# Performance work log

Hardware: AMD Instinct MI355X
Metric: run time of the kernel (lower is better)

The kernel has to match this reference:

```python
import jax, jax.numpy as jnp
import numpy as np

B, S, D, H = 2, 2048, 1024, 16
HD = D // H


def setup_inputs() -> dict:
    key = jax.random.key(0)
    ks = jax.random.split(key, 12)
    s = 1.0 / np.sqrt(D)
    inp = {
        "queries": jax.random.normal(ks[0], (B, S, D), jnp.float32),
        "keys": jax.random.normal(ks[1], (B, S, D), jnp.float32),
        "values": jax.random.normal(ks[2], (B, S, D), jnp.float32),
        # True = masked out (causal upper triangle)
        "attn_mask": jnp.triu(jnp.ones((S, S), bool), k=1),
        "W_q": jax.random.normal(ks[3], (D, D), jnp.float32) * s,
        "b_q": jnp.zeros((D,), jnp.float32),
        "W_k": jax.random.normal(ks[4], (D, D), jnp.float32) * s,
        "b_k": jnp.zeros((D,), jnp.float32),
        "W_v": jax.random.normal(ks[5], (D, D), jnp.float32) * s,
        "b_v": jnp.zeros((D,), jnp.float32),
        "W_o": jax.random.normal(ks[6], (D, D), jnp.float32) * s,
        "b_o": jnp.zeros((D,), jnp.float32),
    }
    return inp


def _split_heads(x):
    b, s, _ = x.shape
    return x.reshape(b, s, H, HD).transpose(0, 2, 1, 3)  # (B,H,S,HD)


def reference(queries, keys, values, attn_mask, W_q, b_q, W_k, b_k, W_v, b_v, W_o, b_o):
    Q = _split_heads(queries @ W_q + b_q)
    K = _split_heads(keys @ W_k + b_k)
    V = _split_heads(values @ W_v + b_v)
    scale = 1.0 / np.sqrt(HD)
    scores = jnp.einsum("bhqd,bhkd->bhqk", Q, K) * scale  # (B,H,S,S)
    scores = jnp.where(attn_mask, jnp.float32(-1e9), scores)
    probs = jax.nn.softmax(scores, axis=-1)
    ctx = jnp.einsum("bhqk,bhkd->bhqd", probs, V)
    ctx = ctx.transpose(0, 2, 1, 3).reshape(queries.shape[0], queries.shape[1], D)
    return ctx @ W_o + b_o
```

## Files before the change

kernel.cpp:

```cpp
#include <hip/hip_runtime.h>
#include <hip/hip_bf16.h>
#include <math.h>

typedef __bf16 bf16x8 __attribute__((ext_vector_type(8)));
typedef float f32x4 __attribute__((ext_vector_type(4)));
typedef unsigned short u16x8 __attribute__((ext_vector_type(8)));
typedef unsigned short u16x4 __attribute__((ext_vector_type(4)));

static __device__ __forceinline__ unsigned short f2bf(float f) {
    union { float f; unsigned u; } v; v.f = f;
    unsigned r = v.u + 0x7fffu + ((v.u >> 16) & 1u);
    return (unsigned short)(r >> 16);
}

static __device__ __forceinline__ float exp2fast(float x) {
    return __builtin_exp2f(x);
}

static __device__ __forceinline__ void gload16(const void* g, void* l) {
    __builtin_amdgcn_global_load_lds((const __attribute__((address_space(1))) unsigned int*)g,
                                     (__attribute__((address_space(3))) unsigned int*)l, 16, 0, 0);
}

#define MFMA16(a, b, c) __builtin_amdgcn_mfma_f32_16x16x32_bf16((a), (b), (c), 0, 0, 0)

static __device__ __forceinline__ bf16x8 frag_swz(const unsigned short* base, int row, int chunk) {
    return *(const bf16x8*)((const char*)base + row * 128 + (((chunk ^ row) & 7) << 4));
}

struct Cv3 { const float* in[3]; unsigned short* out[3]; };

__global__ void conv3_kernel(Cv3 a) {
    const int x = blockIdx.x;
    const int sel = x >> 11;
    const size_t i = (((size_t)(x & 2047)) * 256 + threadIdx.x) * 8;
    const float* in = a.in[sel];
    f32x4 v0 = *(const f32x4*)(in + i);
    f32x4 v1 = *(const f32x4*)(in + i + 4);
    u16x8 o;
#pragma unroll
    for (int j = 0; j < 4; ++j) { o[j] = f2bf(v0[j]); o[j + 4] = f2bf(v1[j]); }
    *(u16x8*)(a.out[sel] + i) = o;
}

struct Cw4 { const float* W[4]; unsigned short* Wt[4]; };

__global__ void conv_wt4_kernel(Cw4 a) {
    __shared__ __align__(16) unsigned short Ws[64][66];
    const float* W = a.W[blockIdx.z];
    unsigned short* Wt = a.Wt[blockIdx.z];
    const int t = threadIdx.x;
    const int r0 = blockIdx.y * 64;
    const int c0 = blockIdx.x * 64;
#pragma unroll
    for (int p = 0; p < 4; ++p) {
        int lin = p * 256 + t;
        int r = lin >> 4, cc = (lin & 15) * 4;
        f32x4 v = *(const f32x4*)(W + (size_t)(r0 + r) * 1024 + c0 + cc);
#pragma unroll
        for (int j = 0; j < 4; ++j) Ws[r][cc + j] = f2bf(v[j]);
    }
    __syncthreads();
#pragma unroll
    for (int p = 0; p < 2; ++p) {
        int lin = p * 256 + t;
        int n = lin >> 3, kc = (lin & 7) * 8;
        u16x8 o;
#pragma unroll
        for (int j = 0; j < 8; ++j) o[j] = Ws[kc + j][n];
        *(u16x8*)(Wt + (size_t)(c0 + n) * 1024 + r0 + kc) = o;
    }
}

struct QkvArgs {
    const unsigned short* A[3];
    const unsigned short* Wt[3];
    const float* bias[3];
    unsigned short* out[3];
    float scale[3];
};

__global__ __launch_bounds__(256, 3)
void gemm_qkv(QkvArgs p)
{
    __shared__ __align__(16) unsigned short As[128 * 64];
    __shared__ __align__(16) unsigned short Bs[128 * 64];

    const int z = blockIdx.z;
    const unsigned short* A  = p.A[z];
    const unsigned short* Bt = p.Wt[z];
    const float* bias = p.bias[z];
    unsigned short* out = p.out[z];
    const float oscale = p.scale[z];

    const int t = threadIdx.x, lane = t & 63, w = t >> 6;
    const int lr = lane & 15, lh = lane >> 4;
    const int m0 = blockIdx.y * 128, n0 = blockIdx.x * 128;
    const int wm = (w >> 1) * 64, wn = (w & 1) * 64;
    const int wbase = (t & 0xC0) * 8;

    f32x4 acc[4][4];
#pragma unroll
    for (int i = 0; i < 4; ++i)
#pragma unroll
        for (int j = 0; j < 4; ++j)
#pragma unroll
            for (int e = 0; e < 4; ++e) acc[i][j][e] = 0.0f;

    for (int kt = 0; kt < 16; ++kt) {
        const int k0 = kt << 6;
        __syncthreads();
#pragma unroll
        for (int q = 0; q < 4; ++q) {
            int lin = q * 256 + t;
            int row = lin >> 3, sc = (lin ^ (lin >> 3)) & 7;
            gload16(A + (size_t)(m0 + row) * 1024 + k0 + sc * 8, &As[q * 2048 + wbase]);
        }
#pragma unroll
        for (int q = 0; q < 4; ++q) {
            int lin = q * 256 + t;
            int row = lin >> 3, sc = (lin ^ (lin >> 3)) & 7;
            gload16(Bt + (size_t)(n0 + row) * 1024 + k0 + sc * 8, &Bs[q * 2048 + wbase]);
        }
        __syncthreads();
#pragma unroll
        for (int kb = 0; kb < 2; ++kb) {
            bf16x8 a[4], b[4];
#pragma unroll
            for (int i = 0; i < 4; ++i) a[i] = frag_swz(As, wm + i * 16 + lr, kb * 4 + lh);
#pragma unroll
            for (int j = 0; j < 4; ++j) b[j] = frag_swz(Bs, wn + j * 16 + lr, kb * 4 + lh);
#pragma unroll
            for (int i = 0; i < 4; ++i)
#pragma unroll
                for (int j = 0; j < 4; ++j)
                    acc[i][j] = MFMA16(a[i], b[j], acc[i][j]);
        }
    }

#pragma unroll
    for (int i = 0; i < 4; ++i) {
#pragma unroll
        for (int j = 0; j < 4; ++j) {
            const int gcol = n0 + wn + j * 16 + lr;
            const float bv = bias[gcol];
            const int h_ = gcol >> 6, hd_ = gcol & 63;
            if (z == 2) {
                const int grow0 = m0 + wm + i * 16 + lh * 4;
                const int b_ = grow0 >> 11, s_ = grow0 & 2047;
                u16x4 pk;
#pragma unroll
                for (int r = 0; r < 4; ++r) pk[r] = f2bf((acc[i][j][r] + bv) * oscale);
                *(u16x4*)(out + (((size_t)((b_ * 16 + h_) * 64 + hd_)) << 11) + s_) = pk;
            } else {
#pragma unroll
                for (int r = 0; r < 4; ++r) {
                    const int grow = m0 + wm + i * 16 + lh * 4 + r;
                    const int b_ = grow >> 11, s_ = grow & 2047;
                    out[((size_t)((b_ * 16 + h_) * 2048 + s_) << 6) + hd_] =
                        f2bf((acc[i][j][r] + bv) * oscale);
                }
            }
        }
    }
}

__global__ __launch_bounds__(256, 3)
void gemm_o(const unsigned short* __restrict__ A, const unsigned short* __restrict__ Bt,
            const float* __restrict__ bias, float* __restrict__ Out)
{
    __shared__ __align__(16) unsigned short As[2][64 * 64];
    __shared__ __align__(16) unsigned short Bs[2][128 * 64];

    const int t = threadIdx.x, lane = t & 63, w = t >> 6;
    const int lr = lane & 15, lh = lane >> 4;
    const int m0 = blockIdx.y * 64, n0 = blockIdx.x * 128;
    const int wm = (w >> 1) * 32, wn = (w & 1) * 64;
    const int wbase = (t & 0xC0) * 8;

    f32x4 acc[2][4];
#pragma unroll
    for (int i = 0; i < 2; ++i)
#pragma unroll
        for (int j = 0; j < 4; ++j)
#pragma unroll
            for (int e = 0; e < 4; ++e) acc[i][j][e] = 0.0f;

    auto stage = [&](int buf, int kt) {
        const int k0 = kt << 6;
#pragma unroll
        for (int q = 0; q < 2; ++q) {
            int lin = q * 256 + t;
            int row = lin >> 3, sc = (lin ^ (lin >> 3)) & 7;
            gload16(A + (size_t)(m0 + row) * 1024 + k0 + sc * 8, &As[buf][q * 2048 + wbase]);
        }
#pragma unroll
        for (int q = 0; q < 4; ++q) {
            int lin = q * 256 + t;
            int row = lin >> 3, sc = (lin ^ (lin >> 3)) & 7;
            gload16(Bt + (size_t)(n0 + row) * 1024 + k0 + sc * 8, &Bs[buf][q * 2048 + wbase]);
        }
    };

    stage(0, 0);
    for (int kt = 0; kt < 16; ++kt) {
        __syncthreads();
        if (kt + 1 < 16) stage((kt + 1) & 1, kt + 1);
        const unsigned short* as = As[kt & 1];
        const unsigned short* bs = Bs[kt & 1];
#pragma unroll
        for (int kb = 0; kb < 2; ++kb) {
            bf16x8 a[2], b[4];
#pragma unroll
            for (int i = 0; i < 2; ++i) a[i] = frag_swz(as, wm + i * 16 + lr, kb * 4 + lh);
#pragma unroll
            for (int j = 0; j < 4; ++j) b[j] = frag_swz(bs, wn + j * 16 + lr, kb * 4 + lh);
#pragma unroll
            for (int i = 0; i < 2; ++i)
#pragma unroll
                for (int j = 0; j < 4; ++j)
                    acc[i][j] = MFMA16(a[i], b[j], acc[i][j]);
        }
    }

#pragma unroll
    for (int i = 0; i < 2; ++i) {
#pragma unroll
        for (int j = 0; j < 4; ++j) {
            const int gcol = n0 + wn + j * 16 + lr;
            const float bv = bias[gcol];
#pragma unroll
            for (int r = 0; r < 4; ++r) {
                const int grow = m0 + wm + i * 16 + lh * 4 + r;
                Out[(size_t)grow * 1024 + gcol] = acc[i][j][r] + bv;
            }
        }
    }
}

__global__ __launch_bounds__(256, 2)
void attn_kernel(const unsigned short* __restrict__ Qp,
                 const unsigned short* __restrict__ Kp,
                 const unsigned short* __restrict__ Vtp,
                 unsigned short* __restrict__ Cp)
{
    __shared__ __align__(16) unsigned short Ks[2][64 * 64];
    __shared__ __align__(16) unsigned short Vs[2][64 * 64];
    __shared__ __align__(16) unsigned short Pl[4][16 * 64];

    const int t = threadIdx.x, lane = t & 63, w = t >> 6;
    const int lr = lane & 15, lh = lane >> 4;
    const int wbase = (t & 0xC0) * 8;

    const int g = blockIdx.x;
    const int local = g >> 3;
    const int bh = (g & 7) * 4 + (local >> 4);
    const int qA = local & 15;
    const size_t baseQK = (size_t)bh * (2048 * 64);
    const size_t baseV  = (size_t)bh * (64 * 2048);

    auto stageKV = [&](int buf, int kv0) {
#pragma unroll
        for (int q = 0; q < 2; ++q) {
            int lin = q * 256 + t;
            int row = lin >> 3, sc = (lin ^ (lin >> 3)) & 7;
            gload16(Kp + baseQK + (size_t)(kv0 + row) * 64 + sc * 8, &Ks[buf][q * 2048 + wbase]);
        }
#pragma unroll
        for (int q = 0; q < 2; ++q) {
            int lin = q * 256 + t;
            int row = lin >> 3, sc = (lin ^ (lin >> 3)) & 7;
            gload16(Vtp + baseV + (size_t)row * 2048 + kv0 + sc * 8, &Vs[buf][q * 2048 + wbase]);
        }
    };

    unsigned short* pl = &Pl[w][0];
    const int b_ = bh >> 4, h_ = bh & 15;

    for (int qi = 0; qi < 2; ++qi) {
        const int qt = qi ? (31 - qA) : qA;
        const int q0w = qt * 64 + w * 16;
        const int ntiles = qt + 1;

        const unsigned short* qrow = Qp + baseQK + (size_t)(q0w + lr) * 64 + lh * 8;
        const bf16x8 qf0 = *(const bf16x8*)qrow;
        const bf16x8 qf1 = *(const bf16x8*)(qrow + 32);

        f32x4 o[4]; float m[4], l[4];
#pragma unroll
        for (int i = 0; i < 4; ++i) {
#pragma unroll
            for (int e = 0; e < 4; ++e) o[i][e] = 0.0f;
            m[i] = -INFINITY; l[i] = 0.0f;
        }

        __syncthreads();
        stageKV(0, 0);
        for (int tt = 0; tt < ntiles; ++tt) {
            __syncthreads();
            if (tt + 1 < ntiles) stageKV((tt + 1) & 1, (tt + 1) * 64);
            const unsigned short* ks = Ks[tt & 1];
            const unsigned short* vs = Vs[tt & 1];

            f32x4 s[4];
#pragma unroll
            for (int c = 0; c < 4; ++c) {
#pragma unroll
                for (int e = 0; e < 4; ++e) s[c][e] = 0.0f;
                s[c] = MFMA16(qf0, frag_swz(ks, c * 16 + lr, lh), s[c]);
                s[c] = MFMA16(qf1, frag_swz(ks, c * 16 + lr, 4 + lh), s[c]);
            }

            const bool diag = (tt == qt);
            const int kv0 = tt * 64;
#pragma unroll
            for (int r = 0; r < 4; ++r) {
                const int row = lh * 4 + r;
                const int grow = q0w + row;
                float tv[4];
#pragma unroll
                for (int c = 0; c < 4; ++c) {
                    float x = s[c][r];
                    if (diag && (kv0 + c * 16 + lr > grow)) x = -1e30f;
                    tv[c] = x;
                }
                const float lmax = fmaxf(fmaxf(tv[0], tv[1]), fmaxf(tv[2], tv[3]));
                if (!__all(lmax <= m[r] + 11.0f)) {
                    float cm = lmax;
                    cm = fmaxf(cm, __shfl_xor(cm, 1));
                    cm = fmaxf(cm, __shfl_xor(cm, 2));
                    cm = fmaxf(cm, __shfl_xor(cm, 4));
                    cm = fmaxf(cm, __shfl_xor(cm, 8));
                    const float mn = fmaxf(m[r], cm);
                    const float al = exp2fast(m[r] - mn);
#pragma unroll
                    for (int hc = 0; hc < 4; ++hc) o[hc][r] *= al;
                    l[r] *= al;
                    m[r] = mn;
                }
                float rs = 0.0f;
#pragma unroll
                for (int c = 0; c < 4; ++c) {
                    const float pv = exp2fast(tv[c] - m[r]);
                    rs += pv;
                    *(__bf16*)((char*)pl + row * 128 +
                        ((c * 32 + lr * 2) ^ ((row & 7) << 4))) = (__bf16)pv;
                }
                l[r] += rs;
            }

            const bf16x8 pf0 = frag_swz(pl, lr, lh);
            const bf16x8 pf1 = frag_swz(pl, lr, 4 + lh);
#pragma unroll
            for (int hc = 0; hc < 4; ++hc) {
                o[hc] = MFMA16(pf0, frag_swz(vs, hc * 16 + lr, lh), o[hc]);
                o[hc] = MFMA16(pf1, frag_swz(vs, hc * 16 + lr, 4 + lh), o[hc]);
            }
        }

#pragma unroll
        for (int r = 0; r < 4; ++r) {
            float sum = l[r];
            sum += __shfl_xor(sum, 1);
            sum += __shfl_xor(sum, 2);
            sum += __shfl_xor(sum, 4);
            sum += __shfl_xor(sum, 8);
            const float inv = 1.0f / sum;
            const int srow = q0w + lh * 4 + r;
#pragma unroll
            for (int hc = 0; hc < 4; ++hc) {
                Cp[(size_t)(b_ * 2048 + srow) * 1024 + h_ * 64 + hc * 16 + lr] =
                    f2bf(o[hc][r] * inv);
            }
        }
    }
}

extern "C" void kernel_launch(void* const* d_in, const int* in_sizes, int n_in,
                              void* d_out, int out_size, void* d_ws, size_t ws_size,
                              hipStream_t stream)
{
    const float* queries = (const float*)d_in[0];
    const float* keys    = (const float*)d_in[1];
    const float* values  = (const float*)d_in[2];
    const float* W_q = (const float*)d_in[4];
    const float* b_q = (const float*)d_in[5];
    const float* W_k = (const float*)d_in[6];
    const float* b_k = (const float*)d_in[7];
    const float* W_v = (const float*)d_in[8];
    const float* b_v = (const float*)d_in[9];
    const float* W_o = (const float*)d_in[10];
    const float* b_o = (const float*)d_in[11];

    constexpr size_t NE = (size_t)4 * 1024 * 1024;
    constexpr size_t WE = (size_t)1024 * 1024;
    unsigned short* qc  = (unsigned short*)d_ws;
    unsigned short* kc  = qc + NE;
    unsigned short* vc  = kc + NE;
    unsigned short* wqT = vc + NE;
    unsigned short* wkT = wqT + WE;
    unsigned short* wvT = wkT + WE;
    unsigned short* woT = wvT + WE;
    unsigned short* Qb  = woT + WE;
    unsigned short* Kb  = Qb + NE;
    unsigned short* Vtb = Kb + NE;
    unsigned short* Cb  = Vtb + NE;

    const float qscale = 0.125f * 1.44269504f;

    Cv3 cv;
    cv.in[0] = queries; cv.in[1] = keys; cv.in[2] = values;
    cv.out[0] = qc; cv.out[1] = kc; cv.out[2] = vc;
    conv3_kernel<<<6144, 256, 0, stream>>>(cv);

    Cw4 cw;
    cw.W[0] = W_q; cw.W[1] = W_k; cw.W[2] = W_v; cw.W[3] = W_o;
    cw.Wt[0] = wqT; cw.Wt[1] = wkT; cw.Wt[2] = wvT; cw.Wt[3] = woT;
    conv_wt4_kernel<<<dim3(16, 16, 4), 256, 0, stream>>>(cw);

    QkvArgs qp;
    qp.A[0] = qc;  qp.Wt[0] = wqT; qp.bias[0] = b_q; qp.out[0] = Qb;  qp.scale[0] = qscale;
    qp.A[1] = kc;  qp.Wt[1] = wkT; qp.bias[1] = b_k; qp.out[1] = Kb;  qp.scale[1] = 1.0f;
    qp.A[2] = vc;  qp.Wt[2] = wvT; qp.bias[2] = b_v; qp.out[2] = Vtb; qp.scale[2] = 1.0f;
    gemm_qkv<<<dim3(8, 32, 3), 256, 0, stream>>>(qp);

    attn_kernel<<<512, 256, 0, stream>>>(Qb, Kb, Vtb, Cb);

    gemm_o<<<dim3(8, 64), 256, 0, stream>>>(Cb, woT, b_o, (float*)d_out);
}
```

Before: 245.5 us.

## Fuse prep kernels, restructure attention blocks, split-K output GEMM

The two conversion kernels are merged into one prep launch to save a launch. The attention kernel now uses 512-thread blocks in which two 4-wave groups handle adjacent query tiles and share the K/V staging, replacing the sequential pairing of q-tiles. It also raises MFMA sections to high wave priority. The output projection becomes a split-K GEMM with 128x128 tiles, no double buffering, and an extra add kernel, reusing workspace buffers for the partial results. This trades more launches and extra fp32 traffic for more parallelism, at the risk of workload imbalance in attention because tile pairs now grow with p.

```diff
diff --git a/kernel.cpp b/kernel.cpp
--- a/kernel.cpp
+++ b/kernel.cpp
@@ -28,30 +28,33 @@
     return *(const bf16x8*)((const char*)base + row * 128 + (((chunk ^ row) & 7) << 4));
 }
 
-struct Cv3 { const float* in[3]; unsigned short* out[3]; };
-
-__global__ void conv3_kernel(Cv3 a) {
-    const int x = blockIdx.x;
-    const int sel = x >> 11;
-    const size_t i = (((size_t)(x & 2047)) * 256 + threadIdx.x) * 8;
-    const float* in = a.in[sel];
-    f32x4 v0 = *(const f32x4*)(in + i);
-    f32x4 v1 = *(const f32x4*)(in + i + 4);
-    u16x8 o;
-#pragma unroll
-    for (int j = 0; j < 4; ++j) { o[j] = f2bf(v0[j]); o[j + 4] = f2bf(v1[j]); }
-    *(u16x8*)(a.out[sel] + i) = o;
-}
-
-struct Cw4 { const float* W[4]; unsigned short* Wt[4]; };
-
-__global__ void conv_wt4_kernel(Cw4 a) {
+struct PrepArgs {
+    const float* act[3]; unsigned short* actout[3];
+    const float* W[4];   unsigned short* Wt[4];
+};
+
+__global__ void prep_kernel(PrepArgs a) {
     __shared__ __align__(16) unsigned short Ws[64][66];
-    const float* W = a.W[blockIdx.z];
-    unsigned short* Wt = a.Wt[blockIdx.z];
-    const int t = threadIdx.x;
-    const int r0 = blockIdx.y * 64;
-    const int c0 = blockIdx.x * 64;
+    const int b = blockIdx.x, t = threadIdx.x;
+    if (b < 6144) {
+        const int sel = b >> 11;
+        const size_t i = (((size_t)(b & 2047)) * 256 + t) * 8;
+        const float* in = a.act[sel];
+        f32x4 v0 = *(const f32x4*)(in + i);
+        f32x4 v1 = *(const f32x4*)(in + i + 4);
+        u16x8 o;
+#pragma unroll
+        for (int j = 0; j < 4; ++j) { o[j] = f2bf(v0[j]); o[j + 4] = f2bf(v1[j]); }
+        *(u16x8*)(a.actout[sel] + i) = o;
+        return;
+    }
+    const int idx = b - 6144;
+    const int z = idx >> 8;
+    const int rem = idx & 255;
+    const int c0 = (rem & 15) * 64;
+    const int r0 = (rem >> 4) * 64;
+    const float* W = a.W[z];
+    unsigned short* Wt = a.Wt[z];
 #pragma unroll
     for (int p = 0; p < 4; ++p) {
         int lin = p * 256 + t;
@@ -166,57 +169,54 @@
 }
 
 __global__ __launch_bounds__(256, 3)
-void gemm_o(const unsigned short* __restrict__ A, const unsigned short* __restrict__ Bt,
-            const float* __restrict__ bias, float* __restrict__ Out)
+void gemm_o_half(const unsigned short* __restrict__ A, const unsigned short* __restrict__ Bt,
+                 const float* __restrict__ bias, float* __restrict__ P0, float* __restrict__ P1)
 {
-    __shared__ __align__(16) unsigned short As[2][64 * 64];
-    __shared__ __align__(16) unsigned short Bs[2][128 * 64];
-
+    __shared__ __align__(16) unsigned short As[128 * 64];
+    __shared__ __align__(16) unsigned short Bs[128 * 64];
+
+    const int z = blockIdx.z;
+    float* Part = z ? P1 : P0;
     const int t = threadIdx.x, lane = t & 63, w = t >> 6;
     const int lr = lane & 15, lh = lane >> 4;
-    const int m0 = blockIdx.y * 64, n0 = blockIdx.x * 128;
-    const int wm = (w >> 1) * 32, wn = (w & 1) * 64;
+    const int m0 = blockIdx.y * 128, n0 = blockIdx.x * 128;
+    const int wm = (w >> 1) * 64, wn = (w & 1) * 64;
     const int wbase = (t & 0xC0) * 8;
-
-    f32x4 acc[2][4];
-#pragma unroll
-    for (int i = 0; i < 2; ++i)
+    const int kbase = z << 9;
+
+    f32x4 acc[4][4];
+#pragma unroll
+    for (int i = 0; i < 4; ++i)
 #pragma unroll
         for (int j = 0; j < 4; ++j)
 #pragma unroll
             for (int e = 0; e < 4; ++e) acc[i][j][e] = 0.0f;
 
-    auto stage = [&](int buf, int kt) {
-        const int k0 = kt << 6;
-#pragma unroll
-        for (int q = 0; q < 2; ++q) {
-            int lin = q * 256 + t;
-            int row = lin >> 3, sc = (lin ^ (lin >> 3)) & 7;
-            gload16(A + (size_t)(m0 + row) * 1024 + k0 + sc * 8, &As[buf][q * 2048 + wbase]);
-        }
+    for (int kt = 0; kt < 8; ++kt) {
+        const int k0 = kbase + (kt << 6);
+        __syncthreads();
 #pragma unroll
         for (int q = 0; q < 4; ++q) {
             int lin = q * 256 + t;
             int row = lin >> 3, sc = (lin ^ (lin >> 3)) & 7;
-            gload16(Bt + (size_t)(n0 + row) * 1024 + k0 + sc * 8, &Bs[buf][q * 2048 + wbase]);
-        }
-    };
-
-    stage(0, 0);
-    for (int kt = 0; kt < 16; ++kt) {
+            gload16(A + (size_t)(m0 + row) * 1024 + k0 + sc * 8, &As[q * 2048 + wbase]);
+        }
+#pragma unroll
+        for (int q = 0; q < 4; ++q) {
+            int lin = q * 256 + t;
+            int row = lin >> 3, sc = (lin ^ (lin >> 3)) & 7;
+            gload16(Bt + (size_t)(n0 + row) * 1024 + k0 + sc * 8, &Bs[q * 2048 + wbase]);
+        }
         __syncthreads();
-        if (kt + 1 < 16) stage((kt + 1) & 1, kt + 1);
-        const unsigned short* as = As[kt & 1];
-        const unsigned short* bs = Bs[kt & 1];
 #pragma unroll
         for (int kb = 0; kb < 2; ++kb) {
-            bf16x8 a[2], b[4];
-#pragma unroll
-            for (int i = 0; i < 2; ++i) a[i] = frag_swz(as, wm + i * 16 + lr, kb * 4 + lh);
-#pragma unroll
-            for (int j = 0; j < 4; ++j) b[j] = frag_swz(bs, wn + j * 16 + lr, kb * 4 + lh);
-#pragma unroll
-            for (int i = 0; i < 2; ++i)
+            bf16x8 a[4], b[4];
+#pragma unroll
+            for (int i = 0; i < 4; ++i) a[i] = frag_swz(As, wm + i * 16 + lr, kb * 4 + lh);
+#pragma unroll
+            for (int j = 0; j < 4; ++j) b[j] = frag_swz(Bs, wn + j * 16 + lr, kb * 4 + lh);
+#pragma unroll
+            for (int i = 0; i < 4; ++i)
 #pragma unroll
                 for (int j = 0; j < 4; ++j)
                     acc[i][j] = MFMA16(a[i], b[j], acc[i][j]);
@@ -224,21 +224,32 @@
     }
 
 #pragma unroll
-    for (int i = 0; i < 2; ++i) {
+    for (int i = 0; i < 4; ++i) {
 #pragma unroll
         for (int j = 0; j < 4; ++j) {
             const int gcol = n0 + wn + j * 16 + lr;
-            const float bv = bias[gcol];
+            const float bv = z ? 0.0f : bias[gcol];
 #pragma unroll
             for (int r = 0; r < 4; ++r) {
                 const int grow = m0 + wm + i * 16 + lh * 4 + r;
-                Out[(size_t)grow * 1024 + gcol] = acc[i][j][r] + bv;
+                Part[(size_t)grow * 1024 + gcol] = acc[i][j][r] + bv;
             }
         }
     }
 }
 
-__global__ __launch_bounds__(256, 2)
+__global__ void add2_kernel(const float* __restrict__ P0, const float* __restrict__ P1,
+                            float* __restrict__ out) {
+    const size_t i = ((size_t)blockIdx.x * 256 + threadIdx.x) * 8;
+    f32x4 a0 = *(const f32x4*)(P0 + i),     a1 = *(const f32x4*)(P0 + i + 4);
+    f32x4 b0 = *(const f32x4*)(P1 + i),     b1 = *(const f32x4*)(P1 + i + 4);
+#pragma unroll
+    for (int j = 0; j < 4; ++j) { a0[j] += b0[j]; a1[j] += b1[j]; }
+    *(f32x4*)(out + i) = a0;
+    *(f32x4*)(out + i + 4) = a1;
+}
+
+__global__ __launch_bounds__(512, 4)
 void attn_kernel(const unsigned short* __restrict__ Qp,
                  const unsigned short* __restrict__ Kp,
                  const unsigned short* __restrict__ Vtp,
@@ -246,63 +257,57 @@
 {
     __shared__ __align__(16) unsigned short Ks[2][64 * 64];
     __shared__ __align__(16) unsigned short Vs[2][64 * 64];
-    __shared__ __align__(16) unsigned short Pl[4][16 * 64];
+    __shared__ __align__(16) unsigned short Pl[8][16 * 64];
 
     const int t = threadIdx.x, lane = t & 63, w = t >> 6;
     const int lr = lane & 15, lh = lane >> 4;
-    const int wbase = (t & 0xC0) * 8;
+    const int wbase = (t & 0x1C0) * 8;
 
     const int g = blockIdx.x;
     const int local = g >> 3;
     const int bh = (g & 7) * 4 + (local >> 4);
-    const int qA = local & 15;
+    const int p = local & 15;
+    const int grp = w >> 2;
+    const int qt = 2 * p + grp;
+    const int q0w = qt * 64 + (w & 3) * 16;
+    const int ntiles = 2 * p + 2;
+    const int mytiles = qt + 1;
+
     const size_t baseQK = (size_t)bh * (2048 * 64);
     const size_t baseV  = (size_t)bh * (64 * 2048);
 
     auto stageKV = [&](int buf, int kv0) {
-#pragma unroll
-        for (int q = 0; q < 2; ++q) {
-            int lin = q * 256 + t;
-            int row = lin >> 3, sc = (lin ^ (lin >> 3)) & 7;
-            gload16(Kp + baseQK + (size_t)(kv0 + row) * 64 + sc * 8, &Ks[buf][q * 2048 + wbase]);
-        }
-#pragma unroll
-        for (int q = 0; q < 2; ++q) {
-            int lin = q * 256 + t;
-            int row = lin >> 3, sc = (lin ^ (lin >> 3)) & 7;
-            gload16(Vtp + baseV + (size_t)row * 2048 + kv0 + sc * 8, &Vs[buf][q * 2048 + wbase]);
-        }
+        const int row = t >> 3;
+        const int sc = (t ^ (t >> 3)) & 7;
+        gload16(Kp + baseQK + (size_t)(kv0 + row) * 64 + sc * 8, &Ks[buf][wbase]);
+        gload16(Vtp + baseV + (size_t)row * 2048 + kv0 + sc * 8, &Vs[buf][wbase]);
     };
 
     unsigned short* pl = &Pl[w][0];
     const int b_ = bh >> 4, h_ = bh & 15;
 
-    for (int qi = 0; qi < 2; ++qi) {
-        const int qt = qi ? (31 - qA) : qA;
-        const int q0w = qt * 64 + w * 16;
-        const int ntiles = qt + 1;
-
-        const unsigned short* qrow = Qp + baseQK + (size_t)(q0w + lr) * 64 + lh * 8;
-        const bf16x8 qf0 = *(const bf16x8*)qrow;
-        const bf16x8 qf1 = *(const bf16x8*)(qrow + 32);
-
-        f32x4 o[4]; float m[4], l[4];
-#pragma unroll
-        for (int i = 0; i < 4; ++i) {
-#pragma unroll
-            for (int e = 0; e < 4; ++e) o[i][e] = 0.0f;
-            m[i] = -INFINITY; l[i] = 0.0f;
-        }
-
+    const unsigned short* qrow = Qp + baseQK + (size_t)(q0w + lr) * 64 + lh * 8;
+    const bf16x8 qf0 = *(const bf16x8*)qrow;
+    const bf16x8 qf1 = *(const bf16x8*)(qrow + 32);
+
+    f32x4 o[4]; float m[4], l[4];
+#pragma unroll
+    for (int i = 0; i < 4; ++i) {
+#pragma unroll
+        for (int e = 0; e < 4; ++e) o[i][e] = 0.0f;
+        m[i] = -INFINITY; l[i] = 0.0f;
+    }
+
+    stageKV(0, 0);
+    for (int tt = 0; tt < ntiles; ++tt) {
         __syncthreads();
-        stageKV(0, 0);
-        for (int tt = 0; tt < ntiles; ++tt) {
-            __syncthreads();
-            if (tt + 1 < ntiles) stageKV((tt + 1) & 1, (tt + 1) * 64);
+        if (tt + 1 < ntiles) stageKV((tt + 1) & 1, (tt + 1) * 64);
+        if (tt < mytiles) {
             const unsigned short* ks = Ks[tt & 1];
             const unsigned short* vs = Vs[tt & 1];
 
             f32x4 s[4];
+            __builtin_amdgcn_s_setprio(1);
 #pragma unroll
             for (int c = 0; c < 4; ++c) {
 #pragma unroll
@@ -310,6 +315,7 @@
                 s[c] = MFMA16(qf0, frag_swz(ks, c * 16 + lr, lh), s[c]);
                 s[c] = MFMA16(qf1, frag_swz(ks, c * 16 + lr, 4 + lh), s[c]);
             }
+            __builtin_amdgcn_s_setprio(0);
 
             const bool diag = (tt == qt);
             const int kv0 = tt * 64;
@@ -351,27 +357,29 @@
 
             const bf16x8 pf0 = frag_swz(pl, lr, lh);
             const bf16x8 pf1 = frag_swz(pl, lr, 4 + lh);
+            __builtin_amdgcn_s_setprio(1);
 #pragma unroll
             for (int hc = 0; hc < 4; ++hc) {
                 o[hc] = MFMA16(pf0, frag_swz(vs, hc * 16 + lr, lh), o[hc]);
                 o[hc] = MFMA16(pf1, frag_swz(vs, hc * 16 + lr, 4 + lh), o[hc]);
             }
-        }
-
-#pragma unroll
-        for (int r = 0; r < 4; ++r) {
-            float sum = l[r];
-            sum += __shfl_xor(sum, 1);
-            sum += __shfl_xor(sum, 2);
-            sum += __shfl_xor(sum, 4);
-            sum += __shfl_xor(sum, 8);
-            const float inv = 1.0f / sum;
-            const int srow = q0w + lh * 4 + r;
-#pragma unroll
-            for (int hc = 0; hc < 4; ++hc) {
-                Cp[(size_t)(b_ * 2048 + srow) * 1024 + h_ * 64 + hc * 16 + lr] =
-                    f2bf(o[hc][r] * inv);
-            }
+            __builtin_amdgcn_s_setprio(0);
+        }
+    }
+
+#pragma unroll
+    for (int r = 0; r < 4; ++r) {
+        float sum = l[r];
+        sum += __shfl_xor(sum, 1);
+        sum += __shfl_xor(sum, 2);
+        sum += __shfl_xor(sum, 4);
+        sum += __shfl_xor(sum, 8);
+        const float inv = 1.0f / sum;
+        const int srow = q0w + lh * 4 + r;
+#pragma unroll
+        for (int hc = 0; hc < 4; ++hc) {
+            Cp[(size_t)(b_ * 2048 + srow) * 1024 + h_ * 64 + hc * 16 + lr] =
+                f2bf(o[hc][r] * inv);
         }
     }
 }
@@ -405,18 +413,17 @@
     unsigned short* Kb  = Qb + NE;
     unsigned short* Vtb = Kb + NE;
     unsigned short* Cb  = Vtb + NE;
+    float* P0 = (float*)qc;
+    float* P1 = (float*)Qb;
 
     const float qscale = 0.125f * 1.44269504f;
 
-    Cv3 cv;
-    cv.in[0] = queries; cv.in[1] = keys; cv.in[2] = values;
-    cv.out[0] = qc; cv.out[1] = kc; cv.out[2] = vc;
-    conv3_kernel<<<6144, 256, 0, stream>>>(cv);
-
-    Cw4 cw;
-    cw.W[0] = W_q; cw.W[1] = W_k; cw.W[2] = W_v; cw.W[3] = W_o;
-    cw.Wt[0] = wqT; cw.Wt[1] = wkT; cw.Wt[2] = wvT; cw.Wt[3] = woT;
-    conv_wt4_kernel<<<dim3(16, 16, 4), 256, 0, stream>>>(cw);
+    PrepArgs pa;
+    pa.act[0] = queries; pa.act[1] = keys; pa.act[2] = values;
+    pa.actout[0] = qc; pa.actout[1] = kc; pa.actout[2] = vc;
+    pa.W[0] = W_q; pa.W[1] = W_k; pa.W[2] = W_v; pa.W[3] = W_o;
+    pa.Wt[0] = wqT; pa.Wt[1] = wkT; pa.Wt[2] = wvT; pa.Wt[3] = woT;
+    prep_kernel<<<7168, 256, 0, stream>>>(pa);
 
     QkvArgs qp;
     qp.A[0] = qc;  qp.Wt[0] = wqT; qp.bias[0] = b_q; qp.out[0] = Qb;  qp.scale[0] = qscale;
@@ -424,7 +431,8 @@
     qp.A[2] = vc;  qp.Wt[2] = wvT; qp.bias[2] = b_v; qp.out[2] = Vtb; qp.scale[2] = 1.0f;
     gemm_qkv<<<dim3(8, 32, 3), 256, 0, stream>>>(qp);
 
-    attn_kernel<<<512, 256, 0, stream>>>(Qb, Kb, Vtb, Cb);
-
-    gemm_o<<<dim3(8, 64), 256, 0, stream>>>(Cb, woT, b_o, (float*)d_out);
-}
+    attn_kernel<<<512, 512, 0, stream>>>(Qb, Kb, Vtb, Cb);
+
+    gemm_o_half<<<dim3(8, 32, 2), 256, 0, stream>>>(Cb, woT, b_o, P0, P1);
+    add2_kernel<<<2048, 256, 0, stream>>>(P0, P1, (float*)d_out);
+}
```

New measurement: 293.9 us. 1.2x slower.
